# Kernel tuning notes

Hardware: AMD Instinct MI355X
Metric: run time of the kernel (lower is better)

The kernel has to match this reference:

```python
import jax, jax.numpy as jnp
import numpy as np

B, S, HID = 4, 1024, 4096
H, HKV, D = 32, 8, 128
R = 16
THETA = 10000.0
LORA_SCALE = 1.0


def setup_inputs() -> dict:
    key = jax.random.key(0)
    ks = jax.random.split(key, 13)
    w = 0.02  # init scale for stability
    return {
        "hidden_states": jax.random.normal(ks[0], (B, S, HID), jnp.float32),
        "Wq": jax.random.normal(ks[1], (H * D, HID), jnp.float32) * w,
        "Wk": jax.random.normal(ks[2], (HKV * D, HID), jnp.float32) * w,
        "Wv": jax.random.normal(ks[3], (HKV * D, HID), jnp.float32) * w,
        "Wo": jax.random.normal(ks[4], (HID, H * D), jnp.float32) * w,
        "Aq": jax.random.normal(ks[5], (B, R, HID), jnp.float32) * w,
        "Bq": jax.random.normal(ks[6], (B, H * D, R), jnp.float32) * w,
        "Ak": jax.random.normal(ks[7], (B, R, HID), jnp.float32) * w,
        "Bk": jax.random.normal(ks[8], (B, HKV * D, R), jnp.float32) * w,
        "Av": jax.random.normal(ks[9], (B, R, HID), jnp.float32) * w,
        "Bv": jax.random.normal(ks[10], (B, HKV * D, R), jnp.float32) * w,
        "Ao": jax.random.normal(ks[11], (B, R, H * D), jnp.float32) * w,
        "Bo": jax.random.normal(ks[12], (B, HID, R), jnp.float32) * w,
    }


def _lora(x, A, Bm):
    # per-request (batched) LoRA: x:[B,S,in], A:[B,r,in], Bm:[B,out,r]
    t = jnp.einsum("bsi,bri->bsr", x, A)
    return jnp.einsum("bsr,bor->bso", t, Bm) * LORA_SCALE


def _rope_tables(seq_len, head_dim, theta):
    inv_freq = 1.0 / (theta ** (jnp.arange(0, head_dim, 2, dtype=jnp.float32) / head_dim))
    ang = jnp.arange(seq_len, dtype=jnp.float32)[:, None] * inv_freq[None, :]  # [S, D/2]
    return jnp.cos(ang), jnp.sin(ang)


def _apply_rope(x, cos, sin):
    # x: [B,S,h,D]; cos/sin: [S,D/2]
    x1, x2 = jnp.split(x, 2, axis=-1)
    c = cos[None, :, None, :]
    s = sin[None, :, None, :]
    return jnp.concatenate([x1 * c - x2 * s, x2 * c + x1 * s], axis=-1)


def reference(hidden_states, Wq, Wk, Wv, Wo, Aq, Bq, Ak, Bk, Av, Bv, Ao, Bo):
    x = hidden_states
    # base projections + batched LoRA deltas (apply_lora_weight_kvq)
    q = x @ Wq.T + _lora(x, Aq, Bq)                 # [B,S,H*D]
    k = x @ Wk.T + _lora(x, Ak, Bk)                 # [B,S,HKV*D]
    v = x @ Wv.T + _lora(x, Av, Bv)

    q = q.reshape(B, S, H, D)
    k = k.reshape(B, S, HKV, D)
    v = v.reshape(B, S, HKV, D)

    cos, sin = _rope_tables(S, D, THETA)
    q = _apply_rope(q, cos, sin)
    k = _apply_rope(k, cos, sin)

    # GQA: repeat kv heads to match q heads
    rep = H // HKV
    k = jnp.repeat(k, rep, axis=2)                  # [B,S,H,D]
    v = jnp.repeat(v, rep, axis=2)

    scores = jnp.einsum("bqhd,bkhd->bhqk", q, k) / jnp.sqrt(jnp.float32(D))
    causal = jnp.tril(jnp.ones((S, S), dtype=bool))
    scores = jnp.where(causal[None, None], scores, jnp.finfo(scores.dtype).min)
    probs = jax.nn.softmax(scores, axis=-1)
    attn_raw = jnp.einsum("bhqk,bkhd->bqhd", probs, v).reshape(B, S, H * D)

    # out projection + batched LoRA on attn (apply_lora_weight_attn uses attn_raw)
    out = attn_raw @ Wo.T + _lora(attn_raw, Ao, Bo)  # [B,S,HID]
    return out
```

## Files before the change

### kernel.cpp

```cpp
#include <hip/hip_runtime.h>

typedef unsigned short u16;
typedef __attribute__((ext_vector_type(8))) short short8;
typedef __attribute__((ext_vector_type(4))) float f32x4;

#define BB 4
#define SS 1024
#define HIDN 4096
#define HH 32
#define HKV 8
#define DD 128
#define RR 16
#define MM (BB * SS)

__device__ __forceinline__ u16 f2bf(float f) {
    unsigned u = __builtin_bit_cast(unsigned, f);
    unsigned r = u + 0x7FFFu + ((u >> 16) & 1u);
    return (u16)(r >> 16);
}
__device__ __forceinline__ float bf2f(u16 u) {
    unsigned v = ((unsigned)u) << 16;
    return __builtin_bit_cast(float, v);
}
__device__ __forceinline__ void glds16(const u16* g, u16* l) {
    __builtin_amdgcn_global_load_lds((const __attribute__((address_space(1))) unsigned int*)g,
                                     (__attribute__((address_space(3))) unsigned int*)l, 16, 0, 0);
}

__global__ void zero_kernel(float* __restrict__ p, int n) {
    int i = blockIdx.x * blockDim.x + threadIdx.x;
    if (i < n) p[i] = 0.f;
}

__global__ void cast_kernel(const float* __restrict__ src, u16* __restrict__ dst, int n4) {
    int i = blockIdx.x * blockDim.x + threadIdx.x;
    int stride = gridDim.x * blockDim.x;
    for (; i < n4; i += stride) {
        float4 v = reinterpret_cast<const float4*>(src)[i];
        ushort4 o;
        o.x = f2bf(v.x); o.y = f2bf(v.y); o.z = f2bf(v.z); o.w = f2bf(v.w);
        reinterpret_cast<ushort4*>(dst)[i] = o;
    }
}

__global__ void cast_lora_a(const float* __restrict__ src, u16* __restrict__ dst,
                            int perB4, int dstStrideU16, int n4) {
    int i = blockIdx.x * blockDim.x + threadIdx.x;
    int stride = gridDim.x * blockDim.x;
    for (; i < n4; i += stride) {
        int b = i / perB4;
        int w4 = i - b * perB4;
        float4 v = reinterpret_cast<const float4*>(src)[i];
        ushort4 o;
        o.x = f2bf(v.x); o.y = f2bf(v.y); o.z = f2bf(v.z); o.w = f2bf(v.w);
        reinterpret_cast<ushort4*>(dst + (size_t)b * dstStrideU16)[w4] = o;
    }
}

template <int NT>
__global__ __launch_bounds__(256) void lora_mfma(
        const u16* __restrict__ Xb, const u16* __restrict__ Ab, float* __restrict__ T) {
    const int N = NT * 16;
    __shared__ __attribute__((aligned(16))) u16 Xls[128 * 32];
    __shared__ __attribute__((aligned(16))) u16 Als[NT * 16 * 32];
    int tid = threadIdx.x;
    int wave = tid >> 6, lane = tid & 63;
    int quad = lane >> 4, l15 = lane & 15;
    int m0 = blockIdx.y * 128;
    int b = m0 >> 10;
    int k0base = blockIdx.x * (HIDN / 4);
    const u16* Abb = Ab + (size_t)b * N * HIDN;
    f32x4 acc[2][NT] = {};
    int r0 = tid >> 2;
    int c0 = (tid & 3) * 8;
    for (int k0 = k0base; k0 < k0base + HIDN / 4; k0 += 32) {
        *(uint4*)&Xls[r0 * 32 + c0]        = *(const uint4*)&Xb[(size_t)(m0 + r0) * HIDN + k0 + c0];
        *(uint4*)&Xls[(r0 + 64) * 32 + c0] = *(const uint4*)&Xb[(size_t)(m0 + r0 + 64) * HIDN + k0 + c0];
        if (tid < NT * 16 * 4)
            *(uint4*)&Als[r0 * 32 + c0] = *(const uint4*)&Abb[(size_t)r0 * HIDN + k0 + c0];
        __syncthreads();
        short8 xf[2], af[NT];
#pragma unroll
        for (int mi = 0; mi < 2; mi++)
            xf[mi] = *(const short8*)&Xls[(wave * 32 + mi * 16 + l15) * 32 + quad * 8];
#pragma unroll
        for (int nt = 0; nt < NT; nt++)
            af[nt] = *(const short8*)&Als[(nt * 16 + l15) * 32 + quad * 8];
#pragma unroll
        for (int mi = 0; mi < 2; mi++)
#pragma unroll
            for (int nt = 0; nt < NT; nt++)
                acc[mi][nt] = __builtin_amdgcn_mfma_f32_16x16x32_bf16(xf[mi], af[nt], acc[mi][nt], 0, 0, 0);
        __syncthreads();
    }
#pragma unroll
    for (int mi = 0; mi < 2; mi++)
#pragma unroll
        for (int nt = 0; nt < NT; nt++)
#pragma unroll
            for (int r = 0; r < 4; r++) {
                int row = m0 + wave * 32 + mi * 16 + quad * 4 + r;
                atomicAdd(&T[(size_t)row * N + nt * 16 + l15], acc[mi][nt][r]);
            }
}

__global__ __launch_bounds__(256) void gemm_bt_lora(
        const u16* __restrict__ Xb, const u16* __restrict__ Wb,
        const float* __restrict__ T, int ts, const float* __restrict__ Bl,
        void* __restrict__ outp, int N, int out_f32) {
    const int K = HIDN;
    __shared__ __attribute__((aligned(16))) u16 Als[128 * 32];
    __shared__ __attribute__((aligned(16))) u16 Bls[128 * 32];
    int tid = threadIdx.x;
    int wave = tid >> 6, lane = tid & 63;
    int quad = lane >> 4, l15 = lane & 15;
    int wm = wave >> 1, wn = wave & 1;
    int m0 = blockIdx.y * 128, n0 = blockIdx.x * 128;

    f32x4 acc[4][4] = {};
    int arow = wave * 32 + (lane >> 2);
    int achunk = ((lane & 3) ^ ((lane >> 3) & 3)) * 8;
    const u16* gA0 = &Xb[(size_t)(m0 + arow) * K + achunk];
    const u16* gA1 = gA0 + (size_t)16 * K;
    const u16* gB0 = &Wb[(size_t)(n0 + arow) * K + achunk];
    const u16* gB1 = gB0 + (size_t)16 * K;
    u16* lA0 = &Als[wave * 32 * 32];
    u16* lA1 = &Als[(wave * 32 + 16) * 32];
    u16* lB0 = &Bls[wave * 32 * 32];
    u16* lB1 = &Bls[(wave * 32 + 16) * 32];
    int sel = ((l15 >> 1) & 3);

    for (int k0 = 0; k0 < K; k0 += 32) {
        glds16(gA0 + k0, lA0);
        glds16(gA1 + k0, lA1);
        glds16(gB0 + k0, lB0);
        glds16(gB1 + k0, lB1);
        __syncthreads();
        short8 af[4], bfr[4];
#pragma unroll
        for (int mi = 0; mi < 4; mi++)
            af[mi] = *(const short8*)&Als[(wm * 64 + mi * 16 + l15) * 32 + ((quad ^ sel) * 8)];
#pragma unroll
        for (int ni = 0; ni < 4; ni++)
            bfr[ni] = *(const short8*)&Bls[(wn * 64 + ni * 16 + l15) * 32 + ((quad ^ sel) * 8)];
#pragma unroll
        for (int mi = 0; mi < 4; mi++)
#pragma unroll
            for (int ni = 0; ni < 4; ni++)
                acc[mi][ni] = __builtin_amdgcn_mfma_f32_16x16x32_bf16(af[mi], bfr[ni], acc[mi][ni], 0, 0, 0);
        __syncthreads();
    }

    int bidx = m0 >> 10;
    const float* BlB = Bl + (size_t)bidx * N * RR;
#pragma unroll
    for (int mi = 0; mi < 4; mi++) {
#pragma unroll
        for (int r = 0; r < 4; r++) {
            int row = m0 + wm * 64 + mi * 16 + quad * 4 + r;
            const float4* Tr4 = (const float4*)&T[(size_t)row * ts];
            float4 t4[4];
#pragma unroll
            for (int p = 0; p < 4; p++) t4[p] = Tr4[p];
#pragma unroll
            for (int ni = 0; ni < 4; ni++) {
                int col = n0 + wn * 64 + ni * 16 + l15;
                const float4* Bc4 = (const float4*)&BlB[(size_t)col * RR];
                float add = 0.f;
#pragma unroll
                for (int p = 0; p < 4; p++) {
                    float4 b4 = Bc4[p];
                    add += t4[p].x * b4.x + t4[p].y * b4.y + t4[p].z * b4.z + t4[p].w * b4.w;
                }
                float v = acc[mi][ni][r] + add;
                if (out_f32) ((float*)outp)[(size_t)row * N + col] = v;
                else         ((u16*)outp)[(size_t)row * N + col]  = f2bf(v);
            }
        }
    }
}

__global__ void rope_kernel(u16* __restrict__ x, int nh) {
    int idx = blockIdx.x * 256 + threadIdx.x;
    int total = BB * SS * nh * (DD / 2);
    if (idx >= total) return;
    int d = idx & 63;
    int t = idx >> 6;
    int pos = (t / nh) & (SS - 1);
    size_t base = (size_t)t * DD;
    float inv = __expf(-(float)d * (9.210340371976184f / 64.0f));
    float ang = (float)pos * inv;
    float c = cosf(ang), s = sinf(ang);
    float x1 = bf2f(x[base + d]);
    float x2 = bf2f(x[base + 64 + d]);
    x[base + d]      = f2bf(x1 * c - x2 * s);
    x[base + 64 + d] = f2bf(x2 * c + x1 * s);
}

#define KLD 136
#define VTLD 72
#define PLD 72
__global__ __launch_bounds__(256) void flash_kernel(
        const u16* __restrict__ Q, const u16* __restrict__ Kx, const u16* __restrict__ V,
        u16* __restrict__ Oa) {
    __shared__ __attribute__((aligned(16))) u16 Kls[64 * KLD];
    __shared__ __attribute__((aligned(16))) u16 Vt[128 * VTLD];
    __shared__ __attribute__((aligned(16))) u16 Pls[4 * 32 * PLD];
    int tid = threadIdx.x;
    int wave = tid >> 6, lane = tid & 63;
    int quad = lane >> 4, l15 = lane & 15;
    int blk = blockIdx.x;
    int qt = 7 - (blk >> 7);
    int h  = blk & 31;
    int b  = (blk >> 5) & 3;
    int hkv = h >> 2;
    int q0 = qt * 128;
    const float scale = 0.08838834764831845f;

    short8 qf[2][4];
#pragma unroll
    for (int mi = 0; mi < 2; mi++) {
        int qrow = q0 + (wave + 4 * mi) * 16 + l15;
        const u16* qp = Q + ((size_t)(b * SS + qrow) * HH + h) * DD;
#pragma unroll
        for (int kt = 0; kt < 4; kt++) qf[mi][kt] = *(const short8*)&qp[kt * 32 + quad * 8];
    }

    f32x4 oacc[2][8] = {};
    float mrow[2][4], lrow[2][4];
#pragma unroll
    for (int mi = 0; mi < 2; mi++)
#pragma unroll
        for (int r = 0; r < 4; r++) { mrow[mi][r] = -3.0e38f; lrow[mi][r] = 0.f; }

    int krow = tid >> 2;
    int kc   = (tid & 3) * 32;
    int vp   = tid >> 3;
    int vc   = (tid & 7) * 16;

    int nkb = (q0 >> 6) + 2;
    for (int ib = 0; ib < nkb; ib++) {
        int kb = ib * 64;
        const u16* kg = Kx + ((size_t)(b * SS + kb + krow) * HKV + hkv) * DD + kc;
#pragma unroll
        for (int j = 0; j < 4; j++)
            *(uint4*)&Kls[krow * KLD + kc + j * 8] = *(const uint4*)&kg[j * 8];
        const u16* vg0 = V + ((size_t)(b * SS + kb + 2 * vp) * HKV + hkv) * DD + vc;
        const u16* vg1 = vg0 + HKV * DD;
#pragma unroll
        for (int j = 0; j < 2; j++) {
            uint4 a4 = *(const uint4*)&vg0[j * 8];
            uint4 b4 = *(const uint4*)&vg1[j * 8];
            const u16* ap = (const u16*)&a4;
            const u16* bp = (const u16*)&b4;
#pragma unroll
            for (int e = 0; e < 8; e++) {
                unsigned pk = (unsigned)ap[e] | ((unsigned)bp[e] << 16);
                *(unsigned*)&Vt[(size_t)(vc + j * 8 + e) * VTLD + 2 * vp] = pk;
            }
        }
        __syncthreads();

        f32x4 sa[2][4] = {};
#pragma unroll
        for (int nt = 0; nt < 4; nt++) {
            short8 kf[4];
#pragma unroll
            for (int kt = 0; kt < 4; kt++)
                kf[kt] = *(const short8*)&Kls[(nt * 16 + l15) * KLD + kt * 32 + quad * 8];
#pragma unroll
            for (int mi = 0; mi < 2; mi++)
#pragma unroll
                for (int kt = 0; kt < 4; kt++)
                    sa[mi][nt] = __builtin_amdgcn_mfma_f32_16x16x32_bf16(qf[mi][kt], kf[kt], sa[mi][nt], 0, 0, 0);
        }

#pragma unroll
        for (int mi = 0; mi < 2; mi++) {
#pragma unroll
            for (int r = 0; r < 4; r++) {
                int qpos = q0 + (wave + 4 * mi) * 16 + quad * 4 + r;
                float s[4];
#pragma unroll
                for (int nt = 0; nt < 4; nt++) {
                    float v = sa[mi][nt][r] * scale;
                    int kpos = kb + nt * 16 + l15;
                    s[nt] = (kpos > qpos) ? -3.0e38f : v;
                }
                float mx = fmaxf(fmaxf(s[0], s[1]), fmaxf(s[2], s[3]));
#pragma unroll
                for (int off = 1; off < 16; off <<= 1) mx = fmaxf(mx, __shfl_xor(mx, off, 64));
                float mnew = fmaxf(mrow[mi][r], mx);
                float alpha = __expf(mrow[mi][r] - mnew);
                mrow[mi][r] = mnew;
                float sum = 0.f;
#pragma unroll
                for (int nt = 0; nt < 4; nt++) {
                    float e = __expf(s[nt] - mnew);
                    sum += e;
                    Pls[wave * (32 * PLD) + (mi * 16 + quad * 4 + r) * PLD + nt * 16 + l15] = f2bf(e);
                }
#pragma unroll
                for (int off = 1; off < 16; off <<= 1) sum += __shfl_xor(sum, off, 64);
                lrow[mi][r] = lrow[mi][r] * alpha + sum;
#pragma unroll
                for (int dt = 0; dt < 8; dt++) oacc[mi][dt][r] *= alpha;
            }
        }
        __syncthreads();

#pragma unroll
        for (int kt = 0; kt < 2; kt++) {
            short8 pf[2];
#pragma unroll
            for (int mi = 0; mi < 2; mi++)
                pf[mi] = *(const short8*)&Pls[wave * (32 * PLD) + (mi * 16 + l15) * PLD + kt * 32 + quad * 8];
#pragma unroll
            for (int dt = 0; dt < 8; dt++) {
                short8 vf = *(const short8*)&Vt[(size_t)(dt * 16 + l15) * VTLD + kt * 32 + quad * 8];
#pragma unroll
                for (int mi = 0; mi < 2; mi++)
                    oacc[mi][dt] = __builtin_amdgcn_mfma_f32_16x16x32_bf16(pf[mi], vf, oacc[mi][dt], 0, 0, 0);
            }
        }
        __syncthreads();
    }

#pragma unroll
    for (int mi = 0; mi < 2; mi++)
#pragma unroll
        for (int r = 0; r < 4; r++) {
            float inv = 1.0f / lrow[mi][r];
            int orow = q0 + (wave + 4 * mi) * 16 + quad * 4 + r;
            u16* op = Oa + ((size_t)(b * SS + orow) * HH + h) * DD;
#pragma unroll
            for (int dt = 0; dt < 8; dt++)
                op[dt * 16 + l15] = f2bf(oacc[mi][dt][r] * inv);
        }
}

extern "C" void kernel_launch(void* const* d_in, const int* in_sizes, int n_in,
                              void* d_out, int out_size, void* d_ws, size_t ws_size,
                              hipStream_t stream) {
    const float* X  = (const float*)d_in[0];
    const float* Wq = (const float*)d_in[1];
    const float* Wk = (const float*)d_in[2];
    const float* Wv = (const float*)d_in[3];
    const float* Wo = (const float*)d_in[4];
    const float* Aq = (const float*)d_in[5];
    const float* Bq = (const float*)d_in[6];
    const float* Ak = (const float*)d_in[7];
    const float* Bk = (const float*)d_in[8];
    const float* Av = (const float*)d_in[9];
    const float* Bv = (const float*)d_in[10];
    const float* Ao = (const float*)d_in[11];
    const float* Bo = (const float*)d_in[12];

    char* w = (char*)d_ws;
    auto take = [&](size_t bytes) {
        char* p = w;
        w += (bytes + 255) & ~(size_t)255;
        return p;
    };
    u16*   Xb  = (u16*)  take((size_t)MM * HIDN * 2);
    u16*   Wqb = (u16*)  take((size_t)HIDN * HIDN * 2);
    u16*   Wkb = (u16*)  take((size_t)1024 * HIDN * 2);
    u16*   Wvb = (u16*)  take((size_t)1024 * HIDN * 2);
    u16*   Wob = (u16*)  take((size_t)HIDN * HIDN * 2);
    float* Tcat= (float*)take((size_t)MM * 48 * 4);
    float* To  = (float*)take((size_t)MM * 16 * 4);
    u16*   Acat= (u16*)  take((size_t)BB * 48 * HIDN * 2);
    u16*   Aob = (u16*)  take((size_t)BB * 16 * HIDN * 2);
    u16*   qb  = (u16*)  take((size_t)MM * HIDN * 2);
    u16*   kbuf= (u16*)  take((size_t)MM * 1024 * 2);
    u16*   vbuf= (u16*)  take((size_t)MM * 1024 * 2);
    u16*   attn = Xb;

    zero_kernel<<<(MM * 64 + 255) / 256, 256, 0, stream>>>(Tcat, MM * 64);

    cast_kernel<<<2048, 256, 0, stream>>>(X,  Xb,  MM * HIDN / 4);
    cast_kernel<<<2048, 256, 0, stream>>>(Wq, Wqb, HIDN * HIDN / 4);
    cast_kernel<<<1024, 256, 0, stream>>>(Wk, Wkb, 1024 * HIDN / 4);
    cast_kernel<<<1024, 256, 0, stream>>>(Wv, Wvb, 1024 * HIDN / 4);
    cast_kernel<<<2048, 256, 0, stream>>>(Wo, Wob, HIDN * HIDN / 4);
    {
        const int perB4 = 16 * HIDN / 4;
        const int n4 = BB * perB4;
        cast_lora_a<<<256, 256, 0, stream>>>(Aq, Acat,             perB4, 48 * HIDN, n4);
        cast_lora_a<<<256, 256, 0, stream>>>(Ak, Acat + 16 * HIDN, perB4, 48 * HIDN, n4);
        cast_lora_a<<<256, 256, 0, stream>>>(Av, Acat + 32 * HIDN, perB4, 48 * HIDN, n4);
        cast_kernel<<<256, 256, 0, stream>>>(Ao, Aob, BB * 16 * HIDN / 4);
    }

    lora_mfma<3><<<dim3(4, 32), 256, 0, stream>>>(Xb, Acat, Tcat);

    gemm_bt_lora<<<dim3(32, 32), 256, 0, stream>>>(Xb, Wqb, Tcat,      48, Bq, qb,   HIDN, 0);
    gemm_bt_lora<<<dim3(8,  32), 256, 0, stream>>>(Xb, Wkb, Tcat + 16, 48, Bk, kbuf, 1024, 0);
    gemm_bt_lora<<<dim3(8,  32), 256, 0, stream>>>(Xb, Wvb, Tcat + 32, 48, Bv, vbuf, 1024, 0);
    rope_kernel<<<BB * SS * HH * 64 / 256, 256, 0, stream>>>(qb, HH);
    rope_kernel<<<BB * SS * HKV * 64 / 256, 256, 0, stream>>>(kbuf, HKV);
    flash_kernel<<<BB * HH * (SS / 128), 256, 0, stream>>>(qb, kbuf, vbuf, attn);

    lora_mfma<1><<<dim3(4, 32), 256, 0, stream>>>(attn, Aob, To);
    gemm_bt_lora<<<dim3(32, 32), 256, 0, stream>>>(attn, Wob, To, 16, Bo, (void*)d_out, HIDN, 1);
}
```

Measured before the change: 998.2 us.

## Fuse Q/K/V projections into one GEMM and apply LoRA via MFMA

```diff
diff --git a/kernel.cpp b/kernel.cpp
--- a/kernel.cpp
+++ b/kernel.cpp
@@ -12,6 +12,7 @@
 #define DD 128
 #define RR 16
 #define MM (BB * SS)
+#define NQKV 6144
 
 __device__ __forceinline__ u16 f2bf(float f) {
     unsigned u = __builtin_bit_cast(unsigned, f);
@@ -104,10 +105,12 @@
             }
 }
 
-__global__ __launch_bounds__(256) void gemm_bt_lora(
+__global__ __launch_bounds__(256) void gemm_fused(
         const u16* __restrict__ Xb, const u16* __restrict__ Wb,
-        const float* __restrict__ T, int ts, const float* __restrict__ Bl,
-        void* __restrict__ outp, int N, int out_f32) {
+        const float* __restrict__ T, int tstride,
+        const float* __restrict__ Bl0, const float* __restrict__ Bl1, const float* __restrict__ Bl2,
+        int ns0, int ns1, int ns2, int secb0, int secb1,
+        void* __restrict__ outp, int Nout, int out_f32) {
     const int K = HIDN;
     __shared__ __attribute__((aligned(16))) u16 Als[128 * 32];
     __shared__ __attribute__((aligned(16))) u16 Bls[128 * 32];
@@ -116,6 +119,14 @@
     int quad = lane >> 4, l15 = lane & 15;
     int wm = wave >> 1, wn = wave & 1;
     int m0 = blockIdx.y * 128, n0 = blockIdx.x * 128;
+    int b = m0 >> 10;
+
+    int sec = (n0 >= secb0) + (n0 >= secb1);
+    const float* Blp = (sec == 0) ? Bl0 : ((sec == 1) ? Bl1 : Bl2);
+    int nsec = (sec == 0) ? ns0 : ((sec == 1) ? ns1 : ns2);
+    int colbase = (sec == 0) ? 0 : ((sec == 1) ? secb0 : secb1);
+    int toff = sec * 16;
+    const float* BlB = Blp + (size_t)b * nsec * RR;
 
     f32x4 acc[4][4] = {};
     int arow = wave * 32 + (lane >> 2);
@@ -130,64 +141,93 @@
     u16* lB1 = &Bls[(wave * 32 + 16) * 32];
     int sel = ((l15 >> 1) & 3);
 
+    auto compute = [&]() {
+        short8 af[4], bfr[4];
+#pragma unroll
+        for (int mi = 0; mi < 4; mi++)
+            af[mi] = *(const short8*)&Als[(wm * 64 + mi * 16 + l15) * 32 + ((quad ^ sel) * 8)];
+#pragma unroll
+        for (int ni = 0; ni < 4; ni++)
+            bfr[ni] = *(const short8*)&Bls[(wn * 64 + ni * 16 + l15) * 32 + ((quad ^ sel) * 8)];
+#pragma unroll
+        for (int mi = 0; mi < 4; mi++)
+#pragma unroll
+            for (int ni = 0; ni < 4; ni++)
+                acc[mi][ni] = __builtin_amdgcn_mfma_f32_16x16x32_bf16(af[mi], bfr[ni], acc[mi][ni], 0, 0, 0);
+    };
+
     for (int k0 = 0; k0 < K; k0 += 32) {
         glds16(gA0 + k0, lA0);
         glds16(gA1 + k0, lA1);
         glds16(gB0 + k0, lB0);
         glds16(gB1 + k0, lB1);
         __syncthreads();
-        short8 af[4], bfr[4];
-#pragma unroll
-        for (int mi = 0; mi < 4; mi++)
-            af[mi] = *(const short8*)&Als[(wm * 64 + mi * 16 + l15) * 32 + ((quad ^ sel) * 8)];
-#pragma unroll
-        for (int ni = 0; ni < 4; ni++)
-            bfr[ni] = *(const short8*)&Bls[(wn * 64 + ni * 16 + l15) * 32 + ((quad ^ sel) * 8)];
-#pragma unroll
-        for (int mi = 0; mi < 4; mi++)
-#pragma unroll
-            for (int ni = 0; ni < 4; ni++)
-                acc[mi][ni] = __builtin_amdgcn_mfma_f32_16x16x32_bf16(af[mi], bfr[ni], acc[mi][ni], 0, 0, 0);
-        __syncthreads();
-    }
-
-    int bidx = m0 >> 10;
-    const float* BlB = Bl + (size_t)bidx * N * RR;
+        compute();
+        __syncthreads();
+    }
+
+    {
+        int r = tid >> 1;
+        int s = (r >> 1) & 3;
+        short8 z = {0, 0, 0, 0, 0, 0, 0, 0};
+        if ((tid & 1) == 0) {
+            const float* Tr = &T[(size_t)(m0 + r) * tstride + toff];
+            short8 c0v, c1v;
+#pragma unroll
+            for (int e = 0; e < 4; e++) {
+                c0v[e]     = (short)f2bf(Tr[e]);
+                c0v[e + 4] = (short)f2bf(Tr[4 + e]);
+                c1v[e]     = (short)f2bf(Tr[8 + e]);
+                c1v[e + 4] = (short)f2bf(Tr[12 + e]);
+            }
+            *(short8*)&Als[r * 32 + (0 ^ s) * 8] = c0v;
+            *(short8*)&Als[r * 32 + (1 ^ s) * 8] = c1v;
+            *(short8*)&Als[r * 32 + (2 ^ s) * 8] = z;
+            *(short8*)&Als[r * 32 + (3 ^ s) * 8] = z;
+        } else {
+            const float* Br = &BlB[(size_t)(n0 - colbase + r) * RR];
+            short8 c0v, c1v;
+#pragma unroll
+            for (int e = 0; e < 4; e++) {
+                c0v[e]     = (short)f2bf(Br[e]);
+                c0v[e + 4] = (short)f2bf(Br[4 + e]);
+                c1v[e]     = (short)f2bf(Br[8 + e]);
+                c1v[e + 4] = (short)f2bf(Br[12 + e]);
+            }
+            *(short8*)&Bls[r * 32 + (0 ^ s) * 8] = c0v;
+            *(short8*)&Bls[r * 32 + (1 ^ s) * 8] = c1v;
+            *(short8*)&Bls[r * 32 + (2 ^ s) * 8] = z;
+            *(short8*)&Bls[r * 32 + (3 ^ s) * 8] = z;
+        }
+    }
+    __syncthreads();
+    compute();
+
 #pragma unroll
     for (int mi = 0; mi < 4; mi++) {
 #pragma unroll
         for (int r = 0; r < 4; r++) {
             int row = m0 + wm * 64 + mi * 16 + quad * 4 + r;
-            const float4* Tr4 = (const float4*)&T[(size_t)row * ts];
-            float4 t4[4];
-#pragma unroll
-            for (int p = 0; p < 4; p++) t4[p] = Tr4[p];
 #pragma unroll
             for (int ni = 0; ni < 4; ni++) {
                 int col = n0 + wn * 64 + ni * 16 + l15;
-                const float4* Bc4 = (const float4*)&BlB[(size_t)col * RR];
-                float add = 0.f;
-#pragma unroll
-                for (int p = 0; p < 4; p++) {
-                    float4 b4 = Bc4[p];
-                    add += t4[p].x * b4.x + t4[p].y * b4.y + t4[p].z * b4.z + t4[p].w * b4.w;
-                }
-                float v = acc[mi][ni][r] + add;
-                if (out_f32) ((float*)outp)[(size_t)row * N + col] = v;
-                else         ((u16*)outp)[(size_t)row * N + col]  = f2bf(v);
-            }
-        }
-    }
-}
-
-__global__ void rope_kernel(u16* __restrict__ x, int nh) {
+                float v = acc[mi][ni][r];
+                if (out_f32) ((float*)outp)[(size_t)row * Nout + col] = v;
+                else         ((u16*)outp)[(size_t)row * Nout + col]  = f2bf(v);
+            }
+        }
+    }
+}
+
+__global__ void rope_kernel(u16* __restrict__ x, int lognh, int rowstride, int total) {
     int idx = blockIdx.x * 256 + threadIdx.x;
-    int total = BB * SS * nh * (DD / 2);
     if (idx >= total) return;
     int d = idx & 63;
     int t = idx >> 6;
-    int pos = (t / nh) & (SS - 1);
-    size_t base = (size_t)t * DD;
+    int h = t & ((1 << lognh) - 1);
+    int row = t >> lognh;
+    int pos = row & (SS - 1);
+    size_t base = (size_t)row * rowstride + h * DD;
     float inv = __expf(-(float)d * (9.210340371976184f / 64.0f));
     float ang = (float)pos * inv;
     float c = cosf(ang), s = sinf(ang);
@@ -202,7 +242,7 @@
 #define PLD 72
 __global__ __launch_bounds__(256) void flash_kernel(
         const u16* __restrict__ Q, const u16* __restrict__ Kx, const u16* __restrict__ V,
-        u16* __restrict__ Oa) {
+        u16* __restrict__ Oa, int qs, int kvs) {
     __shared__ __attribute__((aligned(16))) u16 Kls[64 * KLD];
     __shared__ __attribute__((aligned(16))) u16 Vt[128 * VTLD];
     __shared__ __attribute__((aligned(16))) u16 Pls[4 * 32 * PLD];
@@ -221,7 +261,7 @@
 #pragma unroll
     for (int mi = 0; mi < 2; mi++) {
         int qrow = q0 + (wave + 4 * mi) * 16 + l15;
-        const u16* qp = Q + ((size_t)(b * SS + qrow) * HH + h) * DD;
+        const u16* qp = Q + (size_t)(b * SS + qrow) * qs + h * DD;
 #pragma unroll
         for (int kt = 0; kt < 4; kt++) qf[mi][kt] = *(const short8*)&qp[kt * 32 + quad * 8];
     }
@@ -241,12 +281,12 @@
     int nkb = (q0 >> 6) + 2;
     for (int ib = 0; ib < nkb; ib++) {
         int kb = ib * 64;
-        const u16* kg = Kx + ((size_t)(b * SS + kb + krow) * HKV + hkv) * DD + kc;
+        const u16* kg = Kx + (size_t)(b * SS + kb + krow) * kvs + hkv * DD + kc;
 #pragma unroll
         for (int j = 0; j < 4; j++)
             *(uint4*)&Kls[krow * KLD + kc + j * 8] = *(const uint4*)&kg[j * 8];
-        const u16* vg0 = V + ((size_t)(b * SS + kb + 2 * vp) * HKV + hkv) * DD + vc;
-        const u16* vg1 = vg0 + HKV * DD;
+        const u16* vg0 = V + (size_t)(b * SS + kb + 2 * vp) * kvs + hkv * DD + vc;
+        const u16* vg1 = vg0 + kvs;
 #pragma unroll
         for (int j = 0; j < 2; j++) {
             uint4 a4 = *(const uint4*)&vg0[j * 8];
@@ -371,10 +411,10 @@
     float* To  = (float*)take((size_t)MM * 16 * 4);
     u16*   Acat= (u16*)  take((size_t)BB * 48 * HIDN * 2);
     u16*   Aob = (u16*)  take((size_t)BB * 16 * HIDN * 2);
-    u16*   qb  = (u16*)  take((size_t)MM * HIDN * 2);
-    u16*   kbuf= (u16*)  take((size_t)MM * 1024 * 2);
-    u16*   vbuf= (u16*)  take((size_t)MM * 1024 * 2);
+    u16*   qkv = (u16*)  take((size_t)MM * NQKV * 2);
     u16*   attn = Xb;
+
+    (void)Wkb; (void)Wvb;
 
     zero_kernel<<<(MM * 64 + 255) / 256, 256, 0, stream>>>(Tcat, MM * 64);
 
@@ -394,13 +434,18 @@
 
     lora_mfma<3><<<dim3(4, 32), 256, 0, stream>>>(Xb, Acat, Tcat);
 
-    gemm_bt_lora<<<dim3(32, 32), 256, 0, stream>>>(Xb, Wqb, Tcat,      48, Bq, qb,   HIDN, 0);
-    gemm_bt_lora<<<dim3(8,  32), 256, 0, stream>>>(Xb, Wkb, Tcat + 16, 48, Bk, kbuf, 1024, 0);
-    gemm_bt_lora<<<dim3(8,  32), 256, 0, stream>>>(Xb, Wvb, Tcat + 32, 48, Bv, vbuf, 1024, 0);
-    rope_kernel<<<BB * SS * HH * 64 / 256, 256, 0, stream>>>(qb, HH);
-    rope_kernel<<<BB * SS * HKV * 64 / 256, 256, 0, stream>>>(kbuf, HKV);
-    flash_kernel<<<BB * HH * (SS / 128), 256, 0, stream>>>(qb, kbuf, vbuf, attn);
+    gemm_fused<<<dim3(48, 32), 256, 0, stream>>>(
+        Xb, Wqb, Tcat, 48, Bq, Bk, Bv, HIDN, 1024, 1024, 4096, 5120,
+        (void*)qkv, NQKV, 0);
+
+    rope_kernel<<<(BB * SS * HH * 64 + 255) / 256, 256, 0, stream>>>(qkv,        5, NQKV, BB * SS * HH * 64);
+    rope_kernel<<<(BB * SS * HKV * 64 + 255) / 256, 256, 0, stream>>>(qkv + 4096, 3, NQKV, BB * SS * HKV * 64);
+
+    flash_kernel<<<BB * HH * (SS / 128), 256, 0, stream>>>(qkv, qkv + 4096, qkv + 5120, attn, NQKV, NQKV);
 
     lora_mfma<1><<<dim3(4, 32), 256, 0, stream>>>(attn, Aob, To);
-    gemm_bt_lora<<<dim3(32, 32), 256, 0, stream>>>(attn, Wob, To, 16, Bo, (void*)d_out, HIDN, 1);
-}
+
+    gemm_fused<<<dim3(32, 32), 256, 0, stream>>>(
+        attn, Wob, To, 16, Bo, Bo, Bo, HIDN, HIDN, HIDN, 1 << 30, 1 << 30,
+        (void*)d_out, HIDN, 1);
+}
```

After: 904.2 us. 9.4% less time.
